# Optimization experiments

Hardware: AMD Instinct MI355X
Metric: run time of the kernel (lower is better)

Reference implementation:

```python
import jax, jax.numpy as jnp
import numpy as np

B, T, C, H = 4, 2048, 1024, 16
HD = C // H

def setup_inputs() -> dict:
    key = jax.random.key(0)
    ks = jax.random.split(key, 9)
    s = 1.0 / np.sqrt(C)
    return {
        'x':  jax.random.normal(ks[0], (B, T, C), jnp.float32),
        'Wq': jax.random.normal(ks[1], (C, C), jnp.float32) * s,
        'bq': jnp.zeros((C,), jnp.float32),
        'Wk': jax.random.normal(ks[2], (C, C), jnp.float32) * s,
        'bk': jnp.zeros((C,), jnp.float32),
        'Wv': jax.random.normal(ks[3], (C, C), jnp.float32) * s,
        'bv': jnp.zeros((C,), jnp.float32),
        'Wo': jax.random.normal(ks[4], (C, C), jnp.float32) * s,
        'bo': jnp.zeros((C,), jnp.float32),
    }

def reference(x, Wq, bq, Wk, bk, Wv, bv, Wo, bo):
    Bx, Tx, Cx = x.shape
    # projections (torch Linear: x @ W.T + b); split heads -> (B,H,T,HD)
    def heads(y):
        return y.reshape(Bx, Tx, H, HD).transpose(0, 2, 1, 3)
    q = heads(x @ Wq.T + bq)
    k = heads(x @ Wk.T + bk)
    v = heads(x @ Wv.T + bv)
    # NOTE: original scales by 1/sqrt(embedding_dim), not head_dim
    scale = 1.0 / jnp.sqrt(jnp.asarray(Cx, x.dtype))
    att = jnp.einsum('bhqd,bhkd->bhqk', q, k) * scale
    mask = jnp.tril(jnp.ones((Tx, Tx), dtype=bool))
    att = jnp.where(mask, att, jnp.asarray(-jnp.inf, att.dtype))
    att = jax.nn.softmax(att, axis=-1)
    y = jnp.einsum('bhqk,bhkd->bhqd', att, v)
    y = y.transpose(0, 2, 1, 3).reshape(Bx, Tx, Cx)
    return y @ Wo.T + bo
```

## Files before the change

kernel.cpp:

```cpp
#include <hip/hip_runtime.h>
#include <hip/hip_bf16.h>
#include <stdint.h>

#define NB 4
#define NT 2048
#define NC 1024
#define NH 16
#define NHD 64
#define NM (NB*NT)

typedef __attribute__((ext_vector_type(8))) __bf16 bf16x8;
typedef __attribute__((ext_vector_type(4))) float floatx4;
typedef __attribute__((ext_vector_type(4))) unsigned int uintx4;

#define AS1(p) ((const __attribute__((address_space(1))) void*)(p))
#define AS3(p) ((__attribute__((address_space(3))) void*)(p))

__device__ __forceinline__ unsigned short f2bf(float f) {
    union { float f; unsigned int u; } v; v.f = f;
    unsigned int u = v.u;
    return (unsigned short)((u + 0x7FFFu + ((u >> 16) & 1u)) >> 16);
}

__global__ void cast_kernel(const float* __restrict__ in,
                            unsigned short* __restrict__ out, int n4) {
    int i = blockIdx.x * blockDim.x + threadIdx.x;
    if (i >= n4) return;
    floatx4 v = ((const floatx4*)in)[i];
    ushort4 o;
    o.x = f2bf(v.x); o.y = f2bf(v.y); o.z = f2bf(v.z); o.w = f2bf(v.w);
    ((ushort4*)out)[i] = o;
}

__global__ void cast4_kernel(const float* __restrict__ w0, const float* __restrict__ w1,
                             const float* __restrict__ w2, const float* __restrict__ w3,
                             unsigned short* __restrict__ o0, unsigned short* __restrict__ o1,
                             unsigned short* __restrict__ o2, unsigned short* __restrict__ o3,
                             int n4) {
    int i = blockIdx.x * blockDim.x + threadIdx.x;
    if (i >= n4) return;
    const float* in; unsigned short* out;
    switch (blockIdx.y) {
        case 0: in = w0; out = o0; break;
        case 1: in = w1; out = o1; break;
        case 2: in = w2; out = o2; break;
        default: in = w3; out = o3; break;
    }
    floatx4 v = ((const floatx4*)in)[i];
    ushort4 o;
    o.x = f2bf(v.x); o.y = f2bf(v.y); o.z = f2bf(v.z); o.w = f2bf(v.w);
    ((ushort4*)out)[i] = o;
}

#define TM 128
#define TN 128
#define BK 32

__device__ __forceinline__ void gemm_core(
    const unsigned short* __restrict__ A,
    const unsigned short* __restrict__ W,
    const float* __restrict__ bias,
    void* __restrict__ Out,
    unsigned short* As, unsigned short* Bs,
    int m_base, int n_base, int N_out, int K, int mode, float oscale)
{
    const int tid  = threadIdx.x;
    const int lane = tid & 63;
    const int wv   = tid >> 6;
    const int quad = lane >> 4;
    const int l16  = lane & 15;
    const int wm = (wv >> 1) * 64;
    const int wn = (wv & 1) * 64;

    floatx4 acc[4][4];
    #pragma unroll
    for (int i = 0; i < 4; ++i)
        #pragma unroll
        for (int j = 0; j < 4; ++j)
            acc[i][j] = (floatx4){0.f, 0.f, 0.f, 0.f};

    const int srow = lane >> 2;
    const int scol = (lane & 3) * 8;
    const int kTiles = K / BK;

    const unsigned short* Ab = A + (size_t)(m_base + wv*32 + srow) * K + scol;
    const unsigned short* Wb = W + (size_t)(n_base + wv*32 + srow) * K + scol;

    for (int kt = 0; kt < kTiles; ++kt) {
        const int k0 = kt * BK;
        __syncthreads();
        #pragma unroll
        for (int i = 0; i < 2; ++i) {
            const int rb = wv*32 + i*16;
            __builtin_amdgcn_global_load_lds(AS1(Ab + (size_t)i*16*K + k0),
                                             AS3(&As[rb*32]), 16, 0, 0);
            __builtin_amdgcn_global_load_lds(AS1(Wb + (size_t)i*16*K + k0),
                                             AS3(&Bs[rb*32]), 16, 0, 0);
        }
        __syncthreads();

        bf16x8 af[4], bfr[4];
        #pragma unroll
        for (int mi = 0; mi < 4; ++mi)
            af[mi] = *(const bf16x8*)&As[(wm + mi*16 + l16) * 32 + quad*8];
        #pragma unroll
        for (int ni = 0; ni < 4; ++ni)
            bfr[ni] = *(const bf16x8*)&Bs[(wn + ni*16 + l16) * 32 + quad*8];

        #pragma unroll
        for (int mi = 0; mi < 4; ++mi)
            #pragma unroll
            for (int ni = 0; ni < 4; ++ni)
                acc[mi][ni] = __builtin_amdgcn_mfma_f32_16x16x32_bf16(
                    af[mi], bfr[ni], acc[mi][ni], 0, 0, 0);
    }

    #pragma unroll
    for (int mi = 0; mi < 4; ++mi) {
        #pragma unroll
        for (int ni = 0; ni < 4; ++ni) {
            const int col = n_base + wn + ni*16 + l16;
            const float bv = bias[col & 1023];
            #pragma unroll
            for (int r = 0; r < 4; ++r) {
                const int row = m_base + wm + mi*16 + quad*4 + r;
                const float v = (acc[mi][ni][r] + bv) * oscale;
                if (mode == 0) {
                    ((float*)Out)[(size_t)row * N_out + col] = v;
                } else if (mode == 1) {
                    const int bb = row >> 11, t = row & (NT - 1);
                    const int h  = (col >> 6) & (NH - 1), d = col & 63;
                    const int bh = bb * NH + h;
                    const size_t idx =
                        ((size_t)((bh*128 + (t >> 4))*2 + (d >> 5)))*512
                        + (size_t)((((d >> 3) & 3)*16 + (t & 15))*8 + (d & 7));
                    ((unsigned short*)Out)[idx] = f2bf(v);
                } else {
                    const int bb = row >> 11, t = row & (NT - 1);
                    const int h  = (col >> 6) & (NH - 1), hd = col & 63;
                    const int bh = bb * NH + h;
                    const size_t idx =
                        ((size_t)((bh*64 + (t >> 5))*4 + (hd >> 4)))*512
                        + (size_t)((((t >> 3) & 3)*16 + (hd & 15))*8 + (t & 7));
                    ((unsigned short*)Out)[idx] = f2bf(v);
                }
            }
        }
    }
}

#define QSCALE (0.03125f * 1.44269504088896340736f)

__global__ __launch_bounds__(256) void gemm_qkv(
    const unsigned short* __restrict__ A,
    const unsigned short* __restrict__ Wq, const unsigned short* __restrict__ Wk,
    const unsigned short* __restrict__ Wv,
    const float* __restrict__ bq, const float* __restrict__ bk,
    const float* __restrict__ bv,
    unsigned short* __restrict__ Qo, unsigned short* __restrict__ Ko,
    unsigned short* __restrict__ Vo)
{
    __shared__ __align__(16) unsigned short As[TM*BK];
    __shared__ __align__(16) unsigned short Bs[TN*BK];
    const int wi = blockIdx.y >> 3;
    const int n_base = (blockIdx.y & 7) * TN;
    const unsigned short* W; const float* bias; void* Out; int mode; float osc;
    if (wi == 0)      { W = Wq; bias = bq; Out = Qo; mode = 1; osc = QSCALE; }
    else if (wi == 1) { W = Wk; bias = bk; Out = Ko; mode = 1; osc = 1.0f; }
    else              { W = Wv; bias = bv; Out = Vo; mode = 2; osc = 1.0f; }
    gemm_core(A, W, bias, Out, As, Bs, blockIdx.x * TM, n_base, NC, NC, mode, osc);
}

__global__ __launch_bounds__(256) void gemm_out(
    const unsigned short* __restrict__ A,
    const unsigned short* __restrict__ W,
    const float* __restrict__ bias,
    float* __restrict__ Out)
{
    __shared__ __align__(16) unsigned short As[TM*BK];
    __shared__ __align__(16) unsigned short Bs[TN*BK];
    gemm_core(A, W, bias, Out, As, Bs, blockIdx.x * TM, blockIdx.y * TN,
              NC, NC, 0, 1.0f);
}

#define LDPP 68

__device__ __forceinline__ void attn_q32(
    const unsigned short* __restrict__ Qf,
    const unsigned short* __restrict__ Kf,
    const unsigned short* __restrict__ Vf,
    unsigned short* __restrict__ Y,
    unsigned short* Pw, int bh, int st, int lane)
{
    const int quad = lane >> 4, l16 = lane & 15;
    const int q0 = st * 32;
    const int b = bh >> 4, h = bh & (NH - 1);

    const size_t qbase = ((size_t)(bh*128 + st*2))*1024 + (size_t)lane*8;
    const bf16x8 qa0 = *(const bf16x8*)&Qf[qbase];
    const bf16x8 qa1 = *(const bf16x8*)&Qf[qbase + 512];
    const bf16x8 qb0 = *(const bf16x8*)&Qf[qbase + 1024];
    const bf16x8 qb1 = *(const bf16x8*)&Qf[qbase + 1536];

    const unsigned short* kp = Kf + (size_t)bh*131072 + (size_t)lane*8;
    const unsigned short* vp = Vf + (size_t)bh*131072 + (size_t)lane*8;

    floatx4 oa[4], ob[4];
    #pragma unroll
    for (int nt = 0; nt < 4; ++nt) {
        oa[nt] = (floatx4){0.f,0.f,0.f,0.f};
        ob[nt] = (floatx4){0.f,0.f,0.f,0.f};
    }
    float la[4] = {0.f,0.f,0.f,0.f}, lb[4] = {0.f,0.f,0.f,0.f};

    const int ntile = (q0 + 95) >> 6;

    for (int f = 0; f < ntile; ++f) {
        const int j0 = f * 64;
        bf16x8 kf[4][2], vf[4][2];
        {
            const unsigned short* kt = kp + (size_t)(j0 >> 4) * 1024;
            #pragma unroll
            for (int ct = 0; ct < 4; ++ct) {
                kf[ct][0] = *(const bf16x8*)&kt[ct*1024];
                kf[ct][1] = *(const bf16x8*)&kt[ct*1024 + 512];
            }
            const unsigned short* vt = vp + (size_t)(j0 >> 5) * 2048;
            #pragma unroll
            for (int nt = 0; nt < 4; ++nt) {
                vf[nt][0] = *(const bf16x8*)&vt[nt*512];
                vf[nt][1] = *(const bf16x8*)&vt[2048 + nt*512];
            }
        }

        {
            floatx4 s[4];
            #pragma unroll
            for (int ct = 0; ct < 4; ++ct) {
                s[ct] = (floatx4){0.f,0.f,0.f,0.f};
                s[ct] = __builtin_amdgcn_mfma_f32_16x16x32_bf16(qa0, kf[ct][0], s[ct], 0,0,0);
                s[ct] = __builtin_amdgcn_mfma_f32_16x16x32_bf16(qa1, kf[ct][1], s[ct], 0,0,0);
            }
            #pragma unroll
            for (int ct = 0; ct < 4; ++ct)
                #pragma unroll
                for (int r = 0; r < 4; ++r) {
                    const int j   = j0 + ct*16 + l16;
                    const int row = q0 + quad*4 + r;
                    const float p = (j <= row) ? __builtin_amdgcn_exp2f(s[ct][r]) : 0.f;
                    la[r] += p;
                    Pw[(quad*4 + r) * LDPP + ct*16 + l16] = f2bf(p);
                }
            const bf16x8 pf0 = *(const bf16x8*)&Pw[l16 * LDPP + quad*8];
            const bf16x8 pf1 = *(const bf16x8*)&Pw[l16 * LDPP + 32 + quad*8];
            #pragma unroll
            for (int nt = 0; nt < 4; ++nt) {
                oa[nt] = __builtin_amdgcn_mfma_f32_16x16x32_bf16(pf0, vf[nt][0], oa[nt], 0,0,0);
                oa[nt] = __builtin_amdgcn_mfma_f32_16x16x32_bf16(pf1, vf[nt][1], oa[nt], 0,0,0);
            }
        }
        {
            floatx4 s[4];
            #pragma unroll
            for (int ct = 0; ct < 4; ++ct) {
                s[ct] = (floatx4){0.f,0.f,0.f,0.f};
                s[ct] = __builtin_amdgcn_mfma_f32_16x16x32_bf16(qb0, kf[ct][0], s[ct], 0,0,0);
                s[ct] = __builtin_amdgcn_mfma_f32_16x16x32_bf16(qb1, kf[ct][1], s[ct], 0,0,0);
            }
            #pragma unroll
            for (int ct = 0; ct < 4; ++ct)
                #pragma unroll
                for (int r = 0; r < 4; ++r) {
                    const int j   = j0 + ct*16 + l16;
                    const int row = q0 + 16 + quad*4 + r;
                    const float p = (j <= row) ? __builtin_amdgcn_exp2f(s[ct][r]) : 0.f;
                    lb[r] += p;
                    Pw[(quad*4 + r) * LDPP + ct*16 + l16] = f2bf(p);
                }
            const bf16x8 pf0 = *(const bf16x8*)&Pw[l16 * LDPP + quad*8];
            const bf16x8 pf1 = *(const bf16x8*)&Pw[l16 * LDPP + 32 + quad*8];
            #pragma unroll
            for (int nt = 0; nt < 4; ++nt) {
                ob[nt] = __builtin_amdgcn_mfma_f32_16x16x32_bf16(pf0, vf[nt][0], ob[nt], 0,0,0);
                ob[nt] = __builtin_amdgcn_mfma_f32_16x16x32_bf16(pf1, vf[nt][1], ob[nt], 0,0,0);
            }
        }
    }

    #pragma unroll
    for (int r = 0; r < 4; ++r) {
        float x = la[r];
        x += __shfl_xor(x, 1, 16); x += __shfl_xor(x, 2, 16);
        x += __shfl_xor(x, 4, 16); x += __shfl_xor(x, 8, 16);
        la[r] = 1.0f / x;
        float y = lb[r];
        y += __shfl_xor(y, 1, 16); y += __shfl_xor(y, 2, 16);
        y += __shfl_xor(y, 4, 16); y += __shfl_xor(y, 8, 16);
        lb[r] = 1.0f / y;
    }
    #pragma unroll
    for (int nt = 0; nt < 4; ++nt) {
        const int col = h * NHD + nt*16 + l16;
        #pragma unroll
        for (int r = 0; r < 4; ++r) {
            const int rowa = q0 + quad*4 + r;
            Y[((size_t)b * NT + rowa) * NC + col] = f2bf(oa[nt][r] * la[r]);
            Y[((size_t)b * NT + rowa + 16) * NC + col] = f2bf(ob[nt][r] * lb[r]);
        }
    }
}

__global__ __launch_bounds__(256) void flash_attn(
    const unsigned short* __restrict__ Qf,
    const unsigned short* __restrict__ Kf,
    const unsigned short* __restrict__ Vf,
    unsigned short* __restrict__ Y)
{
    __shared__ __align__(16) unsigned short Pl[4][16 * LDPP];
    const int tid  = threadIdx.x;
    const int wave = tid >> 6;
    const int lane = tid & 63;
    const int bh = blockIdx.y;
    const int w = blockIdx.x * 4 + wave;
    unsigned short* Pw = &Pl[wave][0];
    attn_q32(Qf, Kf, Vf, Y, Pw, bh, w, lane);
    attn_q32(Qf, Kf, Vf, Y, Pw, bh, 63 - w, lane);
}

extern "C" void kernel_launch(void* const* d_in, const int* in_sizes, int n_in,
                              void* d_out, int out_size, void* d_ws, size_t ws_size,
                              hipStream_t stream) {
    const float* x  = (const float*)d_in[0];
    const float* Wq = (const float*)d_in[1];
    const float* bq = (const float*)d_in[2];
    const float* Wk = (const float*)d_in[3];
    const float* bk = (const float*)d_in[4];
    const float* Wv = (const float*)d_in[5];
    const float* bv = (const float*)d_in[6];
    const float* Wo = (const float*)d_in[7];
    const float* bo = (const float*)d_in[8];

    char* ws = (char*)d_ws;
    size_t off = 0;
    auto alloc = [&](size_t bytes) -> void* {
        void* p = ws + off;
        off += (bytes + 255) & ~(size_t)255;
        return p;
    };
    unsigned short* xb  = (unsigned short*)alloc((size_t)NM * NC * 2);
    unsigned short* Wqb = (unsigned short*)alloc((size_t)NC * NC * 2);
    unsigned short* Wkb = (unsigned short*)alloc((size_t)NC * NC * 2);
    unsigned short* Wvb = (unsigned short*)alloc((size_t)NC * NC * 2);
    unsigned short* Wob = (unsigned short*)alloc((size_t)NC * NC * 2);
    unsigned short* Qb  = (unsigned short*)alloc((size_t)NM * NC * 2);
    unsigned short* Kb  = (unsigned short*)alloc((size_t)NM * NC * 2);
    unsigned short* Vtb = (unsigned short*)alloc((size_t)NM * NC * 2);
    unsigned short* Yb  = (unsigned short*)alloc((size_t)NM * NC * 2);

    const int nx4 = NM * NC / 4;
    const int nw4 = NC * NC / 4;
    cast_kernel<<<(nx4 + 255)/256, 256, 0, stream>>>(x, xb, nx4);
    cast4_kernel<<<dim3((nw4 + 255)/256, 4), 256, 0, stream>>>(
        Wq, Wk, Wv, Wo, Wqb, Wkb, Wvb, Wob, nw4);

    gemm_qkv<<<dim3(NM / TM, 24), 256, 0, stream>>>(
        xb, Wqb, Wkb, Wvb, bq, bk, bv, Qb, Kb, Vtb);

    flash_attn<<<dim3(8, NB*NH), 256, 0, stream>>>(Qb, Kb, Vtb, Yb);

    gemm_out<<<dim3(NM / TM, NC / TN), 256, 0, stream>>>(Yb, Wob, bo, (float*)d_out);
}
```

Measured before the change: 269.3 us.

## Double GEMM K-tile with fragment-major LDS layout and peel causal diagonal tile

The GEMM core now stages a 64-wide K tile per barrier pair instead of 32. It lays LDS out so each 16-row fragment is contiguous and can be read with one linear lane*8 load, which cuts barrier count per K step and avoids strided LDS reads. The attention loop drops the per-element causal mask test on full off-diagonal tiles and handles only the final diagonal tile with a block-level mask check. The trade-offs are a larger LDS footprint per block and more code from the peeled tail, which may affect occupancy and register pressure.

```diff
diff --git a/kernel.cpp b/kernel.cpp
--- a/kernel.cpp
+++ b/kernel.cpp
@@ -54,7 +54,7 @@
 
 #define TM 128
 #define TN 128
-#define BK 32
+#define BK 64
 
 __device__ __forceinline__ void gemm_core(
     const unsigned short* __restrict__ A,
@@ -79,40 +79,45 @@
         for (int j = 0; j < 4; ++j)
             acc[i][j] = (floatx4){0.f, 0.f, 0.f, 0.f};
 
-    const int srow = lane >> 2;
-    const int scol = (lane & 3) * 8;
     const int kTiles = K / BK;
 
-    const unsigned short* Ab = A + (size_t)(m_base + wv*32 + srow) * K + scol;
-    const unsigned short* Wb = W + (size_t)(n_base + wv*32 + srow) * K + scol;
+    const unsigned short* Ab = A + (size_t)(m_base + wv*32 + l16) * K + quad*8;
+    const unsigned short* Wb = W + (size_t)(n_base + wv*32 + l16) * K + quad*8;
 
     for (int kt = 0; kt < kTiles; ++kt) {
         const int k0 = kt * BK;
         __syncthreads();
         #pragma unroll
         for (int i = 0; i < 2; ++i) {
-            const int rb = wv*32 + i*16;
-            __builtin_amdgcn_global_load_lds(AS1(Ab + (size_t)i*16*K + k0),
-                                             AS3(&As[rb*32]), 16, 0, 0);
-            __builtin_amdgcn_global_load_lds(AS1(Wb + (size_t)i*16*K + k0),
-                                             AS3(&Bs[rb*32]), 16, 0, 0);
+            #pragma unroll
+            for (int kk = 0; kk < 2; ++kk) {
+                __builtin_amdgcn_global_load_lds(
+                    AS1(Ab + (size_t)i*16*K + k0 + kk*32),
+                    AS3(&As[(wv*2 + i)*1024 + kk*512]), 16, 0, 0);
+                __builtin_amdgcn_global_load_lds(
+                    AS1(Wb + (size_t)i*16*K + k0 + kk*32),
+                    AS3(&Bs[(wv*2 + i)*1024 + kk*512]), 16, 0, 0);
+            }
         }
         __syncthreads();
 
-        bf16x8 af[4], bfr[4];
-        #pragma unroll
-        for (int mi = 0; mi < 4; ++mi)
-            af[mi] = *(const bf16x8*)&As[(wm + mi*16 + l16) * 32 + quad*8];
-        #pragma unroll
-        for (int ni = 0; ni < 4; ++ni)
-            bfr[ni] = *(const bf16x8*)&Bs[(wn + ni*16 + l16) * 32 + quad*8];
-
-        #pragma unroll
-        for (int mi = 0; mi < 4; ++mi)
+        #pragma unroll
+        for (int kk = 0; kk < 2; ++kk) {
+            bf16x8 af[4], bfr[4];
+            #pragma unroll
+            for (int mi = 0; mi < 4; ++mi)
+                af[mi] = *(const bf16x8*)&As[((wm >> 4) + mi)*1024 + kk*512 + lane*8];
             #pragma unroll
             for (int ni = 0; ni < 4; ++ni)
-                acc[mi][ni] = __builtin_amdgcn_mfma_f32_16x16x32_bf16(
-                    af[mi], bfr[ni], acc[mi][ni], 0, 0, 0);
+                bfr[ni] = *(const bf16x8*)&Bs[((wn >> 4) + ni)*1024 + kk*512 + lane*8];
+
+            #pragma unroll
+            for (int mi = 0; mi < 4; ++mi)
+                #pragma unroll
+                for (int ni = 0; ni < 4; ++ni)
+                    acc[mi][ni] = __builtin_amdgcn_mfma_f32_16x16x32_bf16(
+                        af[mi], bfr[ni], acc[mi][ni], 0, 0, 0);
+        }
     }
 
     #pragma unroll
@@ -213,9 +218,9 @@
     }
     float la[4] = {0.f,0.f,0.f,0.f}, lb[4] = {0.f,0.f,0.f,0.f};
 
-    const int ntile = (q0 + 95) >> 6;
-
-    for (int f = 0; f < ntile; ++f) {
+    const int Ffull = q0 >> 6;
+
+    for (int f = 0; f < Ffull; ++f) {
         const int j0 = f * 64;
         bf16x8 kf[4][2], vf[4][2];
         {
@@ -232,7 +237,6 @@
                 vf[nt][1] = *(const bf16x8*)&vt[2048 + nt*512];
             }
         }
-
         {
             floatx4 s[4];
             #pragma unroll
@@ -245,9 +249,7 @@
             for (int ct = 0; ct < 4; ++ct)
                 #pragma unroll
                 for (int r = 0; r < 4; ++r) {
-                    const int j   = j0 + ct*16 + l16;
-                    const int row = q0 + quad*4 + r;
-                    const float p = (j <= row) ? __builtin_amdgcn_exp2f(s[ct][r]) : 0.f;
+                    const float p = __builtin_amdgcn_exp2f(s[ct][r]);
                     la[r] += p;
                     Pw[(quad*4 + r) * LDPP + ct*16 + l16] = f2bf(p);
                 }
@@ -271,9 +273,7 @@
             for (int ct = 0; ct < 4; ++ct)
                 #pragma unroll
                 for (int r = 0; r < 4; ++r) {
-                    const int j   = j0 + ct*16 + l16;
-                    const int row = q0 + 16 + quad*4 + r;
-                    const float p = (j <= row) ? __builtin_amdgcn_exp2f(s[ct][r]) : 0.f;
+                    const float p = __builtin_amdgcn_exp2f(s[ct][r]);
                     lb[r] += p;
                     Pw[(quad*4 + r) * LDPP + ct*16 + l16] = f2bf(p);
                 }
@@ -283,6 +283,72 @@
             for (int nt = 0; nt < 4; ++nt) {
                 ob[nt] = __builtin_amdgcn_mfma_f32_16x16x32_bf16(pf0, vf[nt][0], ob[nt], 0,0,0);
                 ob[nt] = __builtin_amdgcn_mfma_f32_16x16x32_bf16(pf1, vf[nt][1], ob[nt], 0,0,0);
+            }
+        }
+    }
+
+    {
+        const int j0 = Ffull * 64;
+        bf16x8 kf[4][2], vf[4][2];
+        {
+            const unsigned short* kt = kp + (size_t)(j0 >> 4) * 1024;
+            #pragma unroll
+            for (int ct = 0; ct < 4; ++ct) {
+                kf[ct][0] = *(const bf16x8*)&kt[ct*1024];
+                kf[ct][1] = *(const bf16x8*)&kt[ct*1024 + 512];
+            }
+            const unsigned short* vt = vp + (size_t)(j0 >> 5) * 2048;
+            #pragma unroll
+            for (int nt = 0; nt < 4; ++nt) {
+                vf[nt][0] = *(const bf16x8*)&vt[nt*512];
+                vf[nt][1] = *(const bf16x8*)&vt[2048 + nt*512];
+            }
+        }
+        #pragma unroll
+        for (int sub = 0; sub < 2; ++sub) {
+            const int row_base = q0 + sub*16;
+            const bf16x8 qx0 = sub ? qb0 : qa0;
+            const bf16x8 qx1 = sub ? qb1 : qa1;
+            float* lx = sub ? lb : la;
+            floatx4* ox = sub ? ob : oa;
+            floatx4 s[4];
+            #pragma unroll
+            for (int ct = 0; ct < 4; ++ct) {
+                s[ct] = (floatx4){0.f,0.f,0.f,0.f};
+                s[ct] = __builtin_amdgcn_mfma_f32_16x16x32_bf16(qx0, kf[ct][0], s[ct], 0,0,0);
+                s[ct] = __builtin_amdgcn_mfma_f32_16x16x32_bf16(qx1, kf[ct][1], s[ct], 0,0,0);
+            }
+            #pragma unroll
+            for (int ct = 0; ct < 4; ++ct) {
+                const int jlo = j0 + ct*16;
+                if (jlo >= row_base + 16) {
+                    #pragma unroll
+                    for (int r = 0; r < 4; ++r)
+                        Pw[(quad*4 + r) * LDPP + ct*16 + l16] = 0;
+                } else if (jlo + 15 <= row_base) {
+                    #pragma unroll
+                    for (int r = 0; r < 4; ++r) {
+                        const float p = __builtin_amdgcn_exp2f(s[ct][r]);
+                        lx[r] += p;
+                        Pw[(quad*4 + r) * LDPP + ct*16 + l16] = f2bf(p);
+                    }
+                } else {
+                    #pragma unroll
+                    for (int r = 0; r < 4; ++r) {
+                        const int j   = jlo + l16;
+                        const int row = row_base + quad*4 + r;
+                        const float p = (j <= row) ? __builtin_amdgcn_exp2f(s[ct][r]) : 0.f;
+                        lx[r] += p;
+                        Pw[(quad*4 + r) * LDPP + ct*16 + l16] = f2bf(p);
+                    }
+                }
+            }
+            const bf16x8 pf0 = *(const bf16x8*)&Pw[l16 * LDPP + quad*8];
+            const bf16x8 pf1 = *(const bf16x8*)&Pw[l16 * LDPP + 32 + quad*8];
+            #pragma unroll
+            for (int nt = 0; nt < 4; ++nt) {
+                ox[nt] = __builtin_amdgcn_mfma_f32_16x16x32_bf16(pf0, vf[nt][0], ox[nt], 0,0,0);
+                ox[nt] = __builtin_amdgcn_mfma_f32_16x16x32_bf16(pf1, vf[nt][1], ox[nt], 0,0,0);
             }
         }
     }
```

Measured after the change: 314.4 us. 16.7% more time.
